# Performance work log

Measured on AMD Instinct MI355X. Metric: run time of the kernel, lower is better.

The kernel has to match this reference:

```python
import jax, jax.numpy as jnp
import numpy as np

B, T, D = 4, 2048, 1024
E, H, K = 8, 2048, 2  # n_expert, expert_dim, top_k


def setup_inputs() -> dict:
    key = jax.random.key(0)
    k1, k2, k3, k4 = jax.random.split(key, 4)
    x = jax.random.normal(k1, (B, T, D), jnp.float32)
    gate_w = jax.random.normal(k2, (D, E), jnp.float32) * 0.02          # Router gate (no bias)
    w1 = jax.random.normal(k3, (E, D, H), jnp.float32) * (1.0 / np.sqrt(D))  # per-expert first Linear
    w2 = jax.random.normal(k4, (E, H, D), jnp.float32) * (1.0 / np.sqrt(H))  # per-expert second Linear
    return {"x": x, "gate_w": gate_w, "w1": w1, "w2": w2}


def reference(x, gate_w, w1, w2):
    b, t, d = x.shape
    xf = x.reshape(-1, d)                                   # [N, D]
    n = xf.shape[0]
    n_expert = gate_w.shape[1]
    # Router
    logits = xf @ gate_w                                    # [N, E]
    probs = jax.nn.softmax(logits, axis=-1)
    topk_probs, topk_idx = jax.lax.top_k(probs, K)          # [N, K]
    topk_probs = topk_probs / jnp.sum(topk_probs, axis=-1, keepdims=True)
    # Dense compute of ALL experts (faithful to original), then gather top-k
    h = jax.nn.gelu(jnp.einsum('nd,edh->neh', xf, w1), approximate=False)  # [N, E, H]
    all_expert_out = jnp.einsum('neh,ehd->ned', h, w2)      # [N, E, D]
    selected = jnp.take_along_axis(all_expert_out, topk_idx[:, :, None], axis=1)  # [N, K, D]
    out = jnp.sum(topk_probs[:, :, None] * selected, axis=1)  # [N, D]  (dropout p=0 -> identity)
    # Load-balancing aux loss
    counts = jnp.zeros((n_expert,), jnp.float32).at[topk_idx.reshape(-1)].add(1.0)
    tokens_per_expert = counts / n
    mean_probs = jnp.mean(probs, axis=0)
    aux_loss = n_expert * jnp.sum(tokens_per_expert * mean_probs)
    return (out.reshape(b, t, d), aux_loss,
            probs.reshape(b, t, n_expert),
            topk_idx.reshape(b, t, K),
            topk_probs.reshape(b, t, K))
```

## Files before the change

### kernel.cpp

```cpp
#include <hip/hip_runtime.h>
#include <hip/hip_bf16.h>
#include <cstdint>

typedef unsigned short u16;
typedef unsigned int u32;
typedef short s16x8 __attribute__((ext_vector_type(8)));
typedef float f32x4 __attribute__((ext_vector_type(4)));

constexpr int NTOK = 8192;
constexpr int DDIM = 1024;
constexpr int NEXP = 8;
constexpr int HDIM = 2048;
constexpr int NPAIR = NTOK * 2;

constexpr size_t OFF_OUT   = 0;
constexpr size_t OFF_AUX   = 8388608;
constexpr size_t OFF_PROBS = 8388609;
constexpr size_t OFF_TIDX  = 8454145;
constexpr size_t OFF_TPR   = 8470529;

constexpr size_t WS_CNT  = 0;
constexpr size_t WS_PSUM = 32;
constexpr size_t WS_IDS  = 1024;
constexpr size_t WS_PRW  = 263168;
constexpr size_t WS_W1T  = 17302528;
constexpr size_t WS_W2T  = 50856960;
constexpr size_t WS_H    = 84411392;
constexpr size_t WS_XG   = 151520256;
constexpr size_t WS_NEED = 185074688;

__device__ __forceinline__ u16 f2b(float f) {
  u32 u = __float_as_uint(f);
  u32 r = (u + 0x7fffu + ((u >> 16) & 1u)) >> 16;
  return (u16)r;
}

typedef const uint32_t __attribute__((address_space(1)))* gptr_t;
typedef uint32_t __attribute__((address_space(3)))* lptr_t;

__device__ __forceinline__ void gload16(const void* gp, void* lp) {
  __builtin_amdgcn_global_load_lds((gptr_t)gp, (lptr_t)(uintptr_t)lp, 16, 0, 0);
}

__global__ __launch_bounds__(256) void prep_kernel(
    const float* __restrict__ x, const float* __restrict__ gw,
    float* __restrict__ outbuf,
    int* __restrict__ cnt, float* __restrict__ psum,
    int* __restrict__ ids, float* __restrict__ prw,
    const float* __restrict__ w1, u16* __restrict__ w1t,
    const float* __restrict__ w2, u16* __restrict__ w2t) {
  __shared__ float smem[DDIM * NEXP];
  __shared__ int lcnt[NEXP];
  __shared__ float psl[NEXP];
  __shared__ int gbl[NEXP];

  const int bid = blockIdx.x;
  const int tid = threadIdx.x;

  if (bid >= 128) {
    int id = bid - 128;
    const float* in;
    u16* out;
    int R, C, e, r;
    if (id < 4096) {
      in = w1; out = w1t; R = DDIM; C = HDIM;
      e = id >> 9; r = id & 511;
    } else {
      id -= 4096;
      in = w2; out = w2t; R = HDIM; C = DDIM;
      e = id >> 9; r = id & 511;
    }
    int xt = (R == DDIM) ? (r & 31) : (r & 15);
    int yt = (R == DDIM) ? (r >> 5) : (r >> 4);
    int c0 = xt * 64, r0 = yt * 64;

    float (*tile)[65] = (float(*)[65])smem;
    int tx = tid & 15, ty = tid >> 4;
    const float* src = in + (size_t)e * R * C;
#pragma unroll
    for (int i = 0; i < 4; ++i) {
      int rr = ty + i * 16;
      float4 v = *(const float4*)(src + (size_t)(r0 + rr) * C + c0 + tx * 4);
      tile[rr][tx * 4 + 0] = v.x; tile[rr][tx * 4 + 1] = v.y;
      tile[rr][tx * 4 + 2] = v.z; tile[rr][tx * 4 + 3] = v.w;
    }
    __syncthreads();
    u16* dst = out + (size_t)e * R * C;
#pragma unroll
    for (int i = 0; i < 4; ++i) {
      int c = ty + i * 16;
      ushort4 o;
      o.x = f2b(tile[tx * 4 + 0][c]); o.y = f2b(tile[tx * 4 + 1][c]);
      o.z = f2b(tile[tx * 4 + 2][c]); o.w = f2b(tile[tx * 4 + 3][c]);
      *(ushort4*)(dst + (size_t)(c0 + c) * R + r0 + tx * 4) = o;
    }
    return;
  }

#pragma unroll
  for (int k = 0; k < 8; ++k)
    ((float4*)smem)[tid + k * 256] = ((const float4*)gw)[tid + k * 256];
  if (tid < NEXP) { lcnt[tid] = 0; psl[tid] = 0.f; }
  __syncthreads();

  const int tloc = tid >> 2, part = tid & 3;
  const int t = bid * 64 + tloc;
  double acc[NEXP];
#pragma unroll
  for (int e = 0; e < NEXP; ++e) acc[e] = 0.0;

  const float* xrow = x + (size_t)t * DDIM + part * 256;
  for (int i = 0; i < 64; ++i) {
    float4 v = ((const float4*)xrow)[i];
    const float* g = &smem[(part * 256 + i * 4) * NEXP];
#pragma unroll
    for (int j = 0; j < 4; ++j) {
      double xs = (double)((const float*)&v)[j];
#pragma unroll
      for (int e = 0; e < NEXP; ++e) acc[e] += xs * (double)g[j * NEXP + e];
    }
  }
#pragma unroll
  for (int e = 0; e < NEXP; ++e) {
    acc[e] += __shfl_xor(acc[e], 1);
    acc[e] += __shfl_xor(acc[e], 2);
  }

  int e0 = 0, e1 = 0, lp0 = 0, lp1 = 0;
  float tp0 = 0.f, tp1 = 0.f;
  if (part == 0) {
    float l[NEXP];
#pragma unroll
    for (int e = 0; e < NEXP; ++e) l[e] = (float)acc[e];
    float m = l[0];
#pragma unroll
    for (int e = 1; e < NEXP; ++e) m = fmaxf(m, l[e]);
    float p[NEXP], s = 0.f;
#pragma unroll
    for (int e = 0; e < NEXP; ++e) { p[e] = expf(l[e] - m); s += p[e]; }
    float inv = 1.0f / s;
#pragma unroll
    for (int e = 0; e < NEXP; ++e) {
      p[e] *= inv;
      outbuf[OFF_PROBS + (size_t)t * NEXP + e] = p[e];
      atomicAdd(&psl[e], p[e]);
    }
#pragma unroll
    for (int e = 1; e < NEXP; ++e) if (p[e] > p[e0]) e0 = e;
    e1 = -1;
#pragma unroll
    for (int e = 0; e < NEXP; ++e)
      if (e != e0 && (e1 < 0 || p[e] > p[e1])) e1 = e;
    float ps = p[e0] + p[e1];
    tp0 = p[e0] / ps;
    tp1 = p[e1] / ps;
    outbuf[OFF_TIDX + t * 2 + 0] = (float)e0;
    outbuf[OFF_TIDX + t * 2 + 1] = (float)e1;
    outbuf[OFF_TPR + t * 2 + 0] = tp0;
    outbuf[OFF_TPR + t * 2 + 1] = tp1;
    lp0 = atomicAdd(&lcnt[e0], 1);
    lp1 = atomicAdd(&lcnt[e1], 1);
  }
  __syncthreads();
  if (tid < NEXP) {
    gbl[tid] = atomicAdd(&cnt[tid], lcnt[tid]);
    atomicAdd(&psum[tid], psl[tid]);
  }
  __syncthreads();
  if (part == 0) {
    int pos0 = gbl[e0] + lp0;
    int pos1 = gbl[e1] + lp1;
    ids[e0 * NTOK + pos0] = t;
    ids[e1 * NTOK + pos1] = t;
    prw[e0 * NTOK + pos0] = tp0;
    prw[e1 * NTOK + pos1] = tp1;
  }
}

__global__ __launch_bounds__(256) void gather_kernel(
    const float* __restrict__ x, u16* __restrict__ xg,
    const int* __restrict__ cnt, const float* __restrict__ psum,
    const int* __restrict__ ids, float* __restrict__ outbuf) {
  const int e = blockIdx.y;
  int cn[NEXP];
#pragma unroll
  for (int i = 0; i < NEXP; ++i) cn[i] = cnt[i];
  int gb = 0;
#pragma unroll
  for (int i = 0; i < NEXP; ++i) if (i < e) gb += cn[i];
  const int cnte = cn[e];

  if (blockIdx.x == 0 && blockIdx.y == 0 && threadIdx.x == 0) {
    float aux = 0.f;
#pragma unroll
    for (int i = 0; i < NEXP; ++i) aux += (float)cn[i] * psum[i];
    outbuf[OFF_AUX] = aux * (float)NEXP / ((float)NTOK * (float)NTOK);
  }

  const int lane = threadIdx.x & 31;
  const int rgrp = threadIdx.x >> 5;
#pragma unroll
  for (int p = 0; p < 8; ++p) {
    int pos = blockIdx.x * 64 + p * 8 + rgrp;
    if (pos < cnte) {
      int tok = ids[e * NTOK + pos];
      const float4* src = (const float4*)(x + (size_t)tok * DDIM);
      ushort4* dst = (ushort4*)(xg + (size_t)(gb + pos) * DDIM);
#pragma unroll
      for (int pp = 0; pp < 8; ++pp) {
        float4 v = src[pp * 32 + lane];
        ushort4 o;
        o.x = f2b(v.x); o.y = f2b(v.y); o.z = f2b(v.z); o.w = f2b(v.w);
        dst[pp * 32 + lane] = o;
      }
    }
  }
}

template <int MODE>
__global__ __launch_bounds__(256, 3) void moe_gemm_kernel(
    const u16* __restrict__ Asrc, const u16* __restrict__ Bt,
    u16* __restrict__ hout, float* __restrict__ yout,
    const int* __restrict__ cnt,
    const int* __restrict__ ids, const float* __restrict__ prw) {
  constexpr int KDIM = (MODE == 0) ? 1024 : 2048;
  constexpr int NDIM = (MODE == 0) ? 2048 : 1024;
  constexpr int NT = KDIM / 32;
  constexpr int NB = NDIM / 128;
  constexpr int MGRP = 4;
  constexpr int QPG = MGRP * NB;
  const int wgid = blockIdx.x;
  const int e = wgid & 7;
  const int q = wgid >> 3;
  const int mg = q / QPG;
  const int r = q % QPG;
  const int m0 = (mg * MGRP + (r % MGRP)) * 128;
  const int n0 = (r / MGRP) * 128;

  int cn[NEXP];
#pragma unroll
  for (int i = 0; i < NEXP; ++i) cn[i] = cnt[i];
  const int cnte = cn[e];
  if (m0 >= cnte) return;
  int gbase = 0;
#pragma unroll
  for (int i = 0; i < NEXP; ++i) if (i < e) gbase += cn[i];

  __shared__ u16 Al[3][128 * 32];
  __shared__ u16 Bl[3][128 * 32];

  const int tid = threadIdx.x;
  const int lane = tid & 63, wid = tid >> 6;
  const int wm = (wid >> 1) * 64, wn = (wid & 1) * 64;
  const int r15 = lane & 15, l4 = lane >> 4;

  const char* aptr[2];
  const char* bptr[2];
#pragma unroll
  for (int qq = 0; qq < 2; ++qq) {
    int j = qq * 256 + tid;
    int row = j >> 2;
    int c = (j & 3) ^ ((row >> 1) & 3);
    int gr = gbase + m0 + row;
    if (gr > NPAIR - 1) gr = NPAIR - 1;
    size_t rowoff = (size_t)gr * KDIM;
    aptr[qq] = (const char*)Asrc + (rowoff + (size_t)c * 8) * 2;
    size_t nrow = (size_t)e * NDIM + n0 + row;
    bptr[qq] = (const char*)Bt + (nrow * KDIM + (size_t)c * 8) * 2;
  }

  f32x4 acc[4][4];
#pragma unroll
  for (int i = 0; i < 4; ++i)
#pragma unroll
    for (int jn = 0; jn < 4; ++jn) acc[i][jn] = (f32x4){0.f, 0.f, 0.f, 0.f};

#define STAGE(b_, kt_)                                                         \
  do {                                                                         \
    const size_t kofs_ = (size_t)(kt_) * 64;               \
    _Pragma("unroll") for (int qq = 0; qq < 2; ++qq) {                         \
      gload16(aptr[qq] + kofs_, (void*)&Al[b_][(size_t)(qq * 256 + tid) * 8]); \
      gload16(bptr[qq] + kofs_, (void*)&Bl[b_][(size_t)(qq * 256 + tid) * 8]); \
    }                                                                          \
  } while (0)

  auto compute = [&](int b) {
    const s16x8* Av = (const s16x8*)Al[b];
    const s16x8* Bv = (const s16x8*)Bl[b];
    s16x8 af[4], bfr[4];
#pragma unroll
    for (int mi = 0; mi < 4; ++mi) {
      int row = wm + mi * 16 + r15;
      af[mi] = Av[row * 4 + (l4 ^ ((row >> 1) & 3))];
    }
#pragma unroll
    for (int ni = 0; ni < 4; ++ni) {
      int row = wn + ni * 16 + r15;
      bfr[ni] = Bv[row * 4 + (l4 ^ ((row >> 1) & 3))];
    }
#pragma unroll
    for (int mi = 0; mi < 4; ++mi)
#pragma unroll
      for (int ni = 0; ni < 4; ++ni)
        acc[mi][ni] = __builtin_amdgcn_mfma_f32_16x16x32_bf16(
            af[mi], bfr[ni], acc[mi][ni], 0, 0, 0);
  };

  STAGE(0, 0);
  STAGE(1, 1);

  int b0 = 0;
  for (int kt = 0; kt < NT; ++kt) {
    if (kt < NT - 1)
      asm volatile("s_waitcnt vmcnt(4)" ::: "memory");
    else
      asm volatile("s_waitcnt vmcnt(0)" ::: "memory");
    __builtin_amdgcn_s_barrier();
    asm volatile("" ::: "memory");
    if (kt + 2 < NT) {
      int bs = b0 + 2; if (bs >= 3) bs -= 3;
      STAGE(bs, kt + 2);
    }
    compute(b0);
    if (++b0 == 3) b0 = 0;
  }
#undef STAGE

#pragma unroll
  for (int mi = 0; mi < 4; ++mi) {
#pragma unroll
    for (int jr = 0; jr < 4; ++jr) {
      int rl = wm + mi * 16 + l4 * 4 + jr;
      if (m0 + rl < cnte) {
        if (MODE == 0) {
          size_t grow = (size_t)(gbase + m0 + rl);
#pragma unroll
          for (int ni = 0; ni < 4; ++ni) {
            float v = acc[mi][ni][jr];
            v = 0.5f * v * (1.0f + erff(v * 0.70710678118654752f));
            int col = n0 + wn + ni * 16 + r15;
            hout[grow * NDIM + col] = f2b(v);
          }
        } else {
          int tok = ids[e * NTOK + m0 + rl];
          float p = prw[e * NTOK + m0 + rl];
#pragma unroll
          for (int ni = 0; ni < 4; ++ni) {
            int col = n0 + wn + ni * 16 + r15;
            atomicAdd(&yout[(size_t)tok * DDIM + col], p * acc[mi][ni][jr]);
          }
        }
      }
    }
  }
}

extern "C" void kernel_launch(void* const* d_in, const int* in_sizes, int n_in,
                              void* d_out, int out_size, void* d_ws, size_t ws_size,
                              hipStream_t stream) {
  const float* x = (const float*)d_in[0];
  const float* gw = (const float*)d_in[1];
  const float* w1 = (const float*)d_in[2];
  const float* w2 = (const float*)d_in[3];
  float* out = (float*)d_out;
  char* w = (char*)d_ws;
  if (ws_size < WS_NEED) return;

  int* cnt = (int*)(w + WS_CNT);
  float* psum = (float*)(w + WS_PSUM);
  int* ids = (int*)(w + WS_IDS);
  float* prw = (float*)(w + WS_PRW);
  u16* w1t = (u16*)(w + WS_W1T);
  u16* w2t = (u16*)(w + WS_W2T);
  u16* hbuf = (u16*)(w + WS_H);
  u16* xg = (u16*)(w + WS_XG);

  (void)hipMemsetAsync(w, 0, 96, stream);
  (void)hipMemsetAsync(out + OFF_OUT, 0, (size_t)NTOK * DDIM * sizeof(float), stream);
  prep_kernel<<<128 + 8192, 256, 0, stream>>>(x, gw, out, cnt, psum, ids, prw,
                                              w1, w1t, w2, w2t);
  gather_kernel<<<dim3(NTOK / 64, NEXP), 256, 0, stream>>>(x, xg, cnt, psum, ids, out);
  moe_gemm_kernel<0><<<NEXP * 64 * (HDIM / 128), 256, 0, stream>>>(
      xg, w1t, hbuf, nullptr, cnt, ids, prw);
  moe_gemm_kernel<1><<<NEXP * 64 * (DDIM / 128), 256, 0, stream>>>(
      hbuf, w2t, nullptr, out + OFF_OUT, cnt, ids, prw);
}
```

Measured before the change: 320.9 us.

## Fuse bf16 conversion into router and gather rows inside first GEMM

The separate gather kernel is removed. The router pass now writes a bf16 copy of x in token order, and the first expert GEMM indexes rows through the routing ids instead of reading a pre-gathered contiguous buffer. The aux-loss write moves into the first GEMM kernel. This saves one launch and roughly halves the activation traffic for the gather. The cost is indirect row addressing in the GEMM A loads, which may reduce locality.

```diff
diff --git a/kernel.cpp b/kernel.cpp
--- a/kernel.cpp
+++ b/kernel.cpp
@@ -26,8 +26,8 @@
 constexpr size_t WS_W1T  = 17302528;
 constexpr size_t WS_W2T  = 50856960;
 constexpr size_t WS_H    = 84411392;
-constexpr size_t WS_XG   = 151520256;
-constexpr size_t WS_NEED = 185074688;
+constexpr size_t WS_XB   = 151520256;
+constexpr size_t WS_NEED = 168297472;
 
 __device__ __forceinline__ u16 f2b(float f) {
   u32 u = __float_as_uint(f);
@@ -46,7 +46,7 @@
     const float* __restrict__ x, const float* __restrict__ gw,
     float* __restrict__ outbuf,
     int* __restrict__ cnt, float* __restrict__ psum,
-    int* __restrict__ ids, float* __restrict__ prw,
+    int* __restrict__ ids, float* __restrict__ prw, u16* __restrict__ xb,
     const float* __restrict__ w1, u16* __restrict__ w1t,
     const float* __restrict__ w2, u16* __restrict__ w2t) {
   __shared__ float smem[DDIM * NEXP];
@@ -110,8 +110,12 @@
   for (int e = 0; e < NEXP; ++e) acc[e] = 0.0;
 
   const float* xrow = x + (size_t)t * DDIM + part * 256;
+  u16* xbrow = xb + (size_t)t * DDIM + part * 256;
   for (int i = 0; i < 64; ++i) {
     float4 v = ((const float4*)xrow)[i];
+    ushort4 o;
+    o.x = f2b(v.x); o.y = f2b(v.y); o.z = f2b(v.z); o.w = f2b(v.w);
+    ((ushort4*)xbrow)[i] = o;
     const float* g = &smem[(part * 256 + i * 4) * NEXP];
 #pragma unroll
     for (int j = 0; j < 4; ++j) {
@@ -177,52 +181,13 @@
   }
 }
 
-__global__ __launch_bounds__(256) void gather_kernel(
-    const float* __restrict__ x, u16* __restrict__ xg,
-    const int* __restrict__ cnt, const float* __restrict__ psum,
-    const int* __restrict__ ids, float* __restrict__ outbuf) {
-  const int e = blockIdx.y;
-  int cn[NEXP];
-#pragma unroll
-  for (int i = 0; i < NEXP; ++i) cn[i] = cnt[i];
-  int gb = 0;
-#pragma unroll
-  for (int i = 0; i < NEXP; ++i) if (i < e) gb += cn[i];
-  const int cnte = cn[e];
-
-  if (blockIdx.x == 0 && blockIdx.y == 0 && threadIdx.x == 0) {
-    float aux = 0.f;
-#pragma unroll
-    for (int i = 0; i < NEXP; ++i) aux += (float)cn[i] * psum[i];
-    outbuf[OFF_AUX] = aux * (float)NEXP / ((float)NTOK * (float)NTOK);
-  }
-
-  const int lane = threadIdx.x & 31;
-  const int rgrp = threadIdx.x >> 5;
-#pragma unroll
-  for (int p = 0; p < 8; ++p) {
-    int pos = blockIdx.x * 64 + p * 8 + rgrp;
-    if (pos < cnte) {
-      int tok = ids[e * NTOK + pos];
-      const float4* src = (const float4*)(x + (size_t)tok * DDIM);
-      ushort4* dst = (ushort4*)(xg + (size_t)(gb + pos) * DDIM);
-#pragma unroll
-      for (int pp = 0; pp < 8; ++pp) {
-        float4 v = src[pp * 32 + lane];
-        ushort4 o;
-        o.x = f2b(v.x); o.y = f2b(v.y); o.z = f2b(v.z); o.w = f2b(v.w);
-        dst[pp * 32 + lane] = o;
-      }
-    }
-  }
-}
-
 template <int MODE>
 __global__ __launch_bounds__(256, 3) void moe_gemm_kernel(
     const u16* __restrict__ Asrc, const u16* __restrict__ Bt,
     u16* __restrict__ hout, float* __restrict__ yout,
-    const int* __restrict__ cnt,
-    const int* __restrict__ ids, const float* __restrict__ prw) {
+    const int* __restrict__ cnt, const float* __restrict__ psum,
+    const int* __restrict__ ids, const float* __restrict__ prw,
+    float* __restrict__ outbuf) {
   constexpr int KDIM = (MODE == 0) ? 1024 : 2048;
   constexpr int NDIM = (MODE == 0) ? 2048 : 1024;
   constexpr int NT = KDIM / 32;
@@ -241,6 +206,14 @@
 #pragma unroll
   for (int i = 0; i < NEXP; ++i) cn[i] = cnt[i];
   const int cnte = cn[e];
+
+  if (MODE == 0 && wgid == 0 && threadIdx.x == 0) {
+    float aux = 0.f;
+#pragma unroll
+    for (int i = 0; i < NEXP; ++i) aux += (float)cn[i] * psum[i];
+    outbuf[OFF_AUX] = aux * (float)NEXP / ((float)NTOK * (float)NTOK);
+  }
+
   if (m0 >= cnte) return;
   int gbase = 0;
 #pragma unroll
@@ -261,9 +234,17 @@
     int j = qq * 256 + tid;
     int row = j >> 2;
     int c = (j & 3) ^ ((row >> 1) & 3);
-    int gr = gbase + m0 + row;
-    if (gr > NPAIR - 1) gr = NPAIR - 1;
-    size_t rowoff = (size_t)gr * KDIM;
+    size_t rowoff;
+    if (MODE == 0) {
+      int mm = m0 + row;
+      if (mm > cnte - 1) mm = cnte - 1;
+      int tok = ids[e * NTOK + mm];
+      rowoff = (size_t)tok * KDIM;
+    } else {
+      int gr = gbase + m0 + row;
+      if (gr > NPAIR - 1) gr = NPAIR - 1;
+      rowoff = (size_t)gr * KDIM;
+    }
     aptr[qq] = (const char*)Asrc + (rowoff + (size_t)c * 8) * 2;
     size_t nrow = (size_t)e * NDIM + n0 + row;
     bptr[qq] = (const char*)Bt + (nrow * KDIM + (size_t)c * 8) * 2;
@@ -373,15 +354,14 @@
   u16* w1t = (u16*)(w + WS_W1T);
   u16* w2t = (u16*)(w + WS_W2T);
   u16* hbuf = (u16*)(w + WS_H);
-  u16* xg = (u16*)(w + WS_XG);
+  u16* xb = (u16*)(w + WS_XB);
 
   (void)hipMemsetAsync(w, 0, 96, stream);
   (void)hipMemsetAsync(out + OFF_OUT, 0, (size_t)NTOK * DDIM * sizeof(float), stream);
-  prep_kernel<<<128 + 8192, 256, 0, stream>>>(x, gw, out, cnt, psum, ids, prw,
+  prep_kernel<<<128 + 8192, 256, 0, stream>>>(x, gw, out, cnt, psum, ids, prw, xb,
                                               w1, w1t, w2, w2t);
-  gather_kernel<<<dim3(NTOK / 64, NEXP), 256, 0, stream>>>(x, xg, cnt, psum, ids, out);
   moe_gemm_kernel<0><<<NEXP * 64 * (HDIM / 128), 256, 0, stream>>>(
-      xg, w1t, hbuf, nullptr, cnt, ids, prw);
+      xb, w1t, hbuf, nullptr, cnt, psum, ids, prw, out);
   moe_gemm_kernel<1><<<NEXP * 64 * (DDIM / 128), 256, 0, stream>>>(
-      hbuf, w2t, nullptr, out + OFF_OUT, cnt, ids, prw);
-}
+      hbuf, w2t, nullptr, out + OFF_OUT, cnt, psum, ids, prw, out);
+}
```

Result: no change. 323.2 us (+0.7%).
